# Kernel tuning notes

Hardware: AMD Instinct MI355X
Metric: run time of the kernel (lower is better)

Reference implementation:

```python
import jax, jax.numpy as jnp
import numpy as np
import math

K_HEADS = 16  # nb_heads from init_kwargs


def setup_inputs() -> dict:
    key = jax.random.key(0)
    ks = jax.random.split(key, 7)
    B, M, H, D = 2, 2048, 1024, 1024 // K_HEADS
    return {
        "h": jax.random.normal(ks[0], (B, M, H), jnp.float32),
        "h_cache": jax.random.normal(ks[1], (B, M, H), jnp.float32),
        "key_pe": jax.random.normal(ks[2], (1, D, M), jnp.float32),
        "Wq": jax.random.normal(ks[3], (H, H), jnp.float32) * 0.02,
        "Wk": jax.random.normal(ks[4], (H, H), jnp.float32) * 0.02,
        "Wv": jax.random.normal(ks[5], (H, H), jnp.float32) * 0.02,
        "Wo": jax.random.normal(ks[6], (H, H), jnp.float32) * 0.02,
    }


def _heads(x, K):
    # [B, M, H] -> [B, K, M, D]
    B, M, H = x.shape
    return x.reshape(B, M, K, H // K).transpose(0, 2, 1, 3)


def reference(h, h_cache, key_pe, Wq, Wk, Wv, Wo):
    B, M, H = h.shape
    K = K_HEADS
    D = H // K
    q = _heads(h @ Wq.T, K)        # [B, K, M, D]
    k = _heads(h_cache @ Wk.T, K)  # [B, K, L, D], L == M
    v = _heads(h_cache @ Wv.T, K)  # [B, K, L, D]

    attn_cont = jnp.einsum("bkmd,bkld->bkml", q, k)            # content scores
    attn_pos = jnp.einsum("bkmd,dl->bkml", q, key_pe[0])       # positional scores
    attn = (attn_cont + attn_pos[..., :M]) / math.sqrt(D)
    attn = jax.nn.softmax(attn, axis=-1)  # computed as in source, but source
    # (faithfully) multiplies VALUE by attn_cont, not attn:
    out = jnp.einsum("bkml,bkld->bkmd", attn_cont, v)          # [B, K, M, D]
    out = out.transpose(0, 2, 1, 3).reshape(B, M, H)
    return out @ Wo.T
```

## Files before the change

kernel.cpp:

```cpp
#include <hip/hip_runtime.h>
#include <hip/hip_bf16.h>

#define BB 2
#define MM 2048
#define HH 1024
#define KH 16

typedef short s16x8 __attribute__((ext_vector_type(8)));
typedef float f32x4 __attribute__((ext_vector_type(4)));
typedef float f32x16 __attribute__((ext_vector_type(16)));

#define GLOBAL_AS __attribute__((address_space(1)))
#define LDS_AS    __attribute__((address_space(3)))

__device__ __forceinline__ void async_copy16(const void* g, void* l) {
    __builtin_amdgcn_global_load_lds((const GLOBAL_AS void*)g, (LDS_AS void*)l, 16, 0, 0);
}

struct __align__(8) bf16x4_t { __hip_bfloat16 x, y, z, w; };

__global__ __launch_bounds__(256) void cvt_all(
    const float* __restrict__ h_f, const float* __restrict__ hc_f,
    const float* __restrict__ Wk_f, const float* __restrict__ Wv_f,
    const float* __restrict__ Wo_f, const float* __restrict__ Wq_f,
    __hip_bfloat16* __restrict__ hb, __hip_bfloat16* __restrict__ hcT,
    __hip_bfloat16* __restrict__ wkb, __hip_bfloat16* __restrict__ wvb,
    __hip_bfloat16* __restrict__ wob, __hip_bfloat16* __restrict__ wqt,
    float* __restrict__ Sz)
{
    __shared__ float Tl[64][65];
    const int seg = blockIdx.y;
    const int t = threadIdx.x;
    const int bx = blockIdx.x;

    if (seg == 1) {
        if (bx >= BB * 512) return;
        const int b = bx >> 9;
        const int tile = bx & 511;
        const int m0 = (tile >> 4) * 64;
        const int k0 = (tile & 15) * 64;
        const int r = t >> 6;
        const int c = t & 63;
        const float* src = hc_f + (size_t)b * MM * HH;
#pragma unroll
        for (int i = 0; i < 64; i += 4)
            Tl[r + i][c] = src[(size_t)(m0 + r + i) * HH + k0 + c];
        __syncthreads();
        __hip_bfloat16* dst = hcT + (size_t)b * HH * MM;
        const int ml = (t & 15) * 4;
#pragma unroll
        for (int ii = 0; ii < 4; ++ii) {
            const int kl = (t >> 4) + 16 * ii;
            bf16x4_t o;
            o.x = __float2bfloat16(Tl[ml + 0][kl]);
            o.y = __float2bfloat16(Tl[ml + 1][kl]);
            o.z = __float2bfloat16(Tl[ml + 2][kl]);
            o.w = __float2bfloat16(Tl[ml + 3][kl]);
            *(bf16x4_t*)(dst + (size_t)(k0 + kl) * MM + m0 + ml) = o;
        }
        return;
    }
    if (seg == 5) {
        if (bx < 128) {
            const int i = (bx * 256 + t) * 4;
            float4 z = {0.f, 0.f, 0.f, 0.f};
            *(float4*)(Sz + i) = z;
            return;
        }
        if (bx >= 384) return;
        const int tile = bx - 128;
        const int j0 = (tile >> 4) * 64;
        const int k0 = (tile & 15) * 64;
        const int r = t >> 6;
        const int c = t & 63;
#pragma unroll
        for (int i = 0; i < 64; i += 4)
            Tl[r + i][c] = Wq_f[(size_t)(j0 + r + i) * HH + k0 + c];
        __syncthreads();
        const int ml = (t & 15) * 4;
#pragma unroll
        for (int ii = 0; ii < 4; ++ii) {
            const int kl = (t >> 4) + 16 * ii;
            bf16x4_t o;
            o.x = __float2bfloat16(Tl[ml + 0][kl]);
            o.y = __float2bfloat16(Tl[ml + 1][kl]);
            o.z = __float2bfloat16(Tl[ml + 2][kl]);
            o.w = __float2bfloat16(Tl[ml + 3][kl]);
            *(bf16x4_t*)(wqt + (size_t)(k0 + kl) * HH + j0 + ml) = o;
        }
        return;
    }
    const float* src;
    __hip_bfloat16* dst;
    int n;
    switch (seg) {
        case 0: src = h_f;  dst = hb;  n = BB * MM * HH; break;
        case 2: src = Wk_f; dst = wkb; n = HH * HH; break;
        case 3: src = Wv_f; dst = wvb; n = HH * HH; break;
        default: src = Wo_f; dst = wob; n = HH * HH; break;
    }
    const int i = (bx * 256 + t) * 4;
    if (i + 3 < n) {
        const float4 v = *(const float4*)(src + i);
        bf16x4_t o;
        o.x = __float2bfloat16(v.x);
        o.y = __float2bfloat16(v.y);
        o.z = __float2bfloat16(v.z);
        o.w = __float2bfloat16(v.w);
        *(bf16x4_t*)(dst + i) = o;
    }
}

__device__ __forceinline__ void store_c(__hip_bfloat16* C, size_t idx, float v) {
    C[idx] = __float2bfloat16(v);
}
__device__ __forceinline__ void store_c(float* C, size_t idx, float v) { C[idx] = v; }

__device__ __forceinline__ f32x16 nt64x2_acc(
    const __hip_bfloat16* __restrict__ A, const __hip_bfloat16* __restrict__ B,
    int kd, size_t ld, __hip_bfloat16* As, __hip_bfloat16* Bs)
{
    const int t    = threadIdx.x;
    const int lane = t & 63;
    const int wave = t >> 6;
    const int srow = lane >> 3;
    const int sw   = ((lane & 7) ^ srow) * 8;
    const int wm   = (wave >> 1) * 32;
    const int wn   = (wave & 1) * 32;
    const int fm   = lane & 31;
    const int fm7  = fm & 7;
    const int ghi  = lane >> 5;

    f32x16 acc = {};
    for (int k0 = 0; k0 < kd; k0 += 128) {
        __syncthreads();
#pragma unroll
        for (int h = 0; h < 2; ++h)
#pragma unroll
            for (int i = 0; i < 2; ++i) {
                const int c = wave * 2 + i;
                async_copy16(A + (size_t)(c * 8 + srow) * ld + k0 + 64 * h + sw,
                             As + h * 4096 + c * 512);
                async_copy16(B + (size_t)(c * 8 + srow) * ld + k0 + 64 * h + sw,
                             Bs + h * 4096 + c * 512);
            }
        __syncthreads();
#pragma unroll
        for (int h = 0; h < 2; ++h)
#pragma unroll
            for (int ks = 0; ks < 64; ks += 16) {
                const int pos = ((((ks >> 3) + ghi) ^ fm7) * 8);
                const s16x8 af = *(const s16x8*)(As + h * 4096 + (wm + fm) * 64 + pos);
                const s16x8 bf = *(const s16x8*)(Bs + h * 4096 + (wn + fm) * 64 + pos);
                acc = __builtin_amdgcn_mfma_f32_32x32x16_bf16(af, bf, acc, 0, 0, 0);
            }
    }
    return acc;
}

template <typename OutT>
__device__ __forceinline__ void store_tile64(OutT* C, int ldc, const f32x16& acc) {
    const int lane = threadIdx.x & 63;
    const int wave = threadIdx.x >> 6;
    const int wm = (wave >> 1) * 32;
    const int wn = (wave & 1) * 32;
    const int col = wn + (lane & 31);
    const int rb  = 4 * (lane >> 5);
#pragma unroll
    for (int r = 0; r < 16; ++r) {
        const int row = wm + (r & 3) + 8 * (r >> 2) + rb;
        store_c(C, (size_t)row * ldc + col, acc[r]);
    }
}

__global__ __launch_bounds__(256) void gemm_g(
    const __hip_bfloat16* __restrict__ hcT, __hip_bfloat16* __restrict__ G)
{
    __shared__ __align__(16) char smem[32768];
    __hip_bfloat16* As = (__hip_bfloat16*)smem;
    __hip_bfloat16* Bs = (__hip_bfloat16*)(smem + 16384);
    __hip_bfloat16* Ts = (__hip_bfloat16*)smem;

    const int b = blockIdx.z;
    int i = 0, rem = blockIdx.x;
    while (rem >= 16 - i) { rem -= 16 - i; ++i; }
    const int j = i + rem;
    const int m0 = i * 64, n0 = j * 64;

    const __hip_bfloat16* Ab = hcT + (size_t)b * HH * MM;
    f32x16 acc = nt64x2_acc(Ab + (size_t)m0 * MM, Ab + (size_t)n0 * MM, MM, MM, As, Bs);

    __hip_bfloat16* Gb = G + (size_t)b * HH * HH;
    store_tile64(Gb + (size_t)m0 * HH + n0, HH, acc);

    if (i == j) return;

    __syncthreads();
    {
        const int lane = threadIdx.x & 63;
        const int wave = threadIdx.x >> 6;
        const int wm = (wave >> 1) * 32;
        const int wn = (wave & 1) * 32;
        const int col = wn + (lane & 31);
        const int rb  = 4 * (lane >> 5);
#pragma unroll
        for (int r = 0; r < 16; ++r) {
            const int row = wm + (r & 3) + 8 * (r >> 2) + rb;
            Ts[row * 72 + col] = __float2bfloat16(acc[r]);
        }
    }
    __syncthreads();
    {
        const int t = threadIdx.x;
        const int rp = t >> 2;
        const int c0 = (t & 3) * 16;
        __hip_bfloat16* dst = Gb + (size_t)(n0 + rp) * HH + m0 + c0;
#pragma unroll
        for (int kk = 0; kk < 4; ++kk) {
            bf16x4_t o;
            o.x = Ts[(c0 + 4 * kk + 0) * 72 + rp];
            o.y = Ts[(c0 + 4 * kk + 1) * 72 + rp];
            o.z = Ts[(c0 + 4 * kk + 2) * 72 + rp];
            o.w = Ts[(c0 + 4 * kk + 3) * 72 + rp];
            *(bf16x4_t*)(dst + 4 * kk) = o;
        }
    }
}

#define LPP 72

__global__ __launch_bounds__(256) void gemm_vt(
    const __hip_bfloat16* __restrict__ wkb, const __hip_bfloat16* __restrict__ wvb,
    const __hip_bfloat16* __restrict__ G, float* __restrict__ S)
{
    __shared__ __align__(16) char smem[32768];
    __hip_bfloat16* As = (__hip_bfloat16*)smem;
    __hip_bfloat16* Bs = (__hip_bfloat16*)(smem + 16384);
    __hip_bfloat16* Pl = (__hip_bfloat16*)smem;
    __hip_bfloat16* Wl = (__hip_bfloat16*)(smem + 64 * LPP * 2);

    const int t    = threadIdx.x;
    const int lane = t & 63;
    const int wave = t >> 6;
    const int kt   = blockIdx.x;
    const int head = blockIdx.y;
    const int b    = blockIdx.z;

    const __hip_bfloat16* Arow = G + (size_t)b * HH * HH + (size_t)kt * 64 * HH;
    const __hip_bfloat16* Brow = wkb + (size_t)head * 64 * HH;

    f32x16 acc = nt64x2_acc(Arow, Brow, HH, HH, As, Bs);
    __syncthreads();

    {
        const int wm = (wave >> 1) * 32;
        const int wn = (wave & 1) * 32;
        const int col_i = wn + (lane & 31);
        const int ghi4  = 4 * (lane >> 5);
#pragma unroll
        for (int g = 0; g < 4; ++g) {
            const int ccb = wm + 8 * g + ghi4;
            bf16x4_t o;
            o.x = __float2bfloat16(acc[4 * g + 0]);
            o.y = __float2bfloat16(acc[4 * g + 1]);
            o.z = __float2bfloat16(acc[4 * g + 2]);
            o.w = __float2bfloat16(acc[4 * g + 3]);
            *(bf16x4_t*)(Pl + col_i * LPP + ccb) = o;
        }
    }
    {
        const int srow = lane >> 3;
        const int sw   = ((lane & 7) ^ srow) * 8;
#pragma unroll
        for (int i = 0; i < 2; ++i) {
            const int c = wave * 2 + i;
            async_copy16(wvb + (size_t)(head * 64 + c * 8 + srow) * HH + kt * 64 + sw,
                         Wl + c * 512);
        }
    }
    __syncthreads();

    const int fr  = lane & 15;
    const int fq  = (lane >> 4) * 8;
    const int wm2 = wave * 16;

    f32x4 acc2[4] = {};
#pragma unroll
    for (int kk = 0; kk < 64; kk += 32) {
        const s16x8 af = *(const s16x8*)(Pl + (wm2 + fr) * LPP + kk + fq);
#pragma unroll
        for (int nj = 0; nj < 4; ++nj) {
            const int row = nj * 16 + fr;
            const s16x8 bfv = *(const s16x8*)(
                Wl + row * 64 + ((((kk + fq) >> 3) ^ (row & 7)) << 3));
            acc2[nj] = __builtin_amdgcn_mfma_f32_16x16x32_bf16(af, bfv, acc2[nj], 0, 0, 0);
        }
    }

    float* Sg = S + ((size_t)b * KH + head) * 4096;
    const int er = (lane >> 4) * 4;
    const int ec = lane & 15;
#pragma unroll
    for (int nj = 0; nj < 4; ++nj)
#pragma unroll
        for (int rr = 0; rr < 4; ++rr)
            atomicAdd(&Sg[(wm2 + er + rr) * 64 + nj * 16 + ec], acc2[nj][rr]);
}

__global__ __launch_bounds__(256) void gemm_f(
    const __hip_bfloat16* __restrict__ W2, const __hip_bfloat16* __restrict__ WqT,
    __hip_bfloat16* __restrict__ F)
{
    __shared__ __align__(16) char smem[32768];
    __hip_bfloat16* As = (__hip_bfloat16*)smem;
    __hip_bfloat16* Bs = (__hip_bfloat16*)(smem + 16384);
    const int b = blockIdx.z;
    const int m0 = blockIdx.x * 64, n0 = blockIdx.y * 64;
    f32x16 acc = nt64x2_acc(W2 + (size_t)b * HH * HH + (size_t)m0 * HH,
                            WqT + (size_t)n0 * HH, HH, HH, As, Bs);
    store_tile64(F + (size_t)b * HH * HH + (size_t)m0 * HH + n0, HH, acc);
}

__global__ __launch_bounds__(256) void gemm_final(
    const __hip_bfloat16* __restrict__ hb, const __hip_bfloat16* __restrict__ F,
    float* __restrict__ outg)
{
    __shared__ __align__(16) char smem[32768];
    __hip_bfloat16* As = (__hip_bfloat16*)smem;
    __hip_bfloat16* Bs = (__hip_bfloat16*)(smem + 16384);
    const int b = blockIdx.z;
    const int m0 = blockIdx.x * 64, n0 = blockIdx.y * 64;
    f32x16 acc = nt64x2_acc(hb + (size_t)b * MM * HH + (size_t)m0 * HH,
                            F + (size_t)b * HH * HH + (size_t)n0 * HH, HH, HH, As, Bs);
    store_tile64(outg + (size_t)b * MM * HH + (size_t)m0 * HH + n0, HH, acc);
}

__global__ __launch_bounds__(256) void w2_fold(
    const __hip_bfloat16* __restrict__ Wo,
    const float* __restrict__ S,
    __hip_bfloat16* __restrict__ W2)
{
    __shared__ float Sl[64 * 68];
    __shared__ float Wl[128 * 68];
    const int t = threadIdx.x, head = blockIdx.y, b = blockIdx.z;
    const int n0 = blockIdx.x * 128;

    const float* Sg = S + ((size_t)b * KH + head) * 4096;
    for (int idx = t; idx < 4096; idx += 256) {
        const int dp = idx >> 6, d = idx & 63;
        Sl[d * 68 + dp] = Sg[idx];
    }
    for (int idx = t; idx < 1024; idx += 256) {
        const int r = idx >> 3, c8 = (idx & 7) * 8;
        s16x8 wv = *(const s16x8*)(Wo + (size_t)(n0 + r) * HH + head * 64 + c8);
#pragma unroll
        for (int j = 0; j < 8; ++j) {
            __hip_bfloat16 wb = *(((const __hip_bfloat16*)&wv) + j);
            Wl[r * 68 + c8 + j] = __bfloat162float(wb);
        }
    }
    __syncthreads();

    const int dpb = (t & 15) * 4;
    const int ng  = t >> 4;
    float acc[8][4] = {};
    for (int d0 = 0; d0 < 64; d0 += 4) {
        f32x4 sv[4];
#pragma unroll
        for (int r = 0; r < 4; ++r)
            sv[r] = *(const f32x4*)(Sl + (d0 + r) * 68 + dpb);
#pragma unroll
        for (int i = 0; i < 8; ++i) {
            const f32x4 wv = *(const f32x4*)(Wl + (ng + 16 * i) * 68 + d0);
#pragma unroll
            for (int r = 0; r < 4; ++r)
#pragma unroll
                for (int j = 0; j < 4; ++j)
                    acc[i][j] += wv[r] * sv[r][j];
        }
    }

#pragma unroll
    for (int i = 0; i < 8; ++i) {
        bf16x4_t o;
        o.x = __float2bfloat16(acc[i][0]);
        o.y = __float2bfloat16(acc[i][1]);
        o.z = __float2bfloat16(acc[i][2]);
        o.w = __float2bfloat16(acc[i][3]);
        *(bf16x4_t*)(W2 + (size_t)b * HH * HH + (size_t)(n0 + ng + 16 * i) * HH
                     + head * 64 + dpb) = o;
    }
}

extern "C" void kernel_launch(void* const* d_in, const int* in_sizes, int n_in,
                              void* d_out, int out_size, void* d_ws, size_t ws_size,
                              hipStream_t stream) {
    const float* h_f  = (const float*)d_in[0];
    const float* hc_f = (const float*)d_in[1];
    const float* Wq_f = (const float*)d_in[3];
    const float* Wk_f = (const float*)d_in[4];
    const float* Wv_f = (const float*)d_in[5];
    const float* Wo_f = (const float*)d_in[6];
    float* out = (float*)d_out;

    const size_t act_b = (size_t)BB * MM * HH * 2;
    const size_t w_b   = (size_t)HH * HH * 2;
    char* ws = (char*)d_ws;
    __hip_bfloat16* hb   = (__hip_bfloat16*)(ws);
    __hip_bfloat16* hcT  = (__hip_bfloat16*)(ws + act_b);
    __hip_bfloat16* wkb  = (__hip_bfloat16*)(ws + 2 * act_b);
    __hip_bfloat16* wvb  = (__hip_bfloat16*)(ws + 2 * act_b + w_b);
    __hip_bfloat16* wob  = (__hip_bfloat16*)(ws + 2 * act_b + 2 * w_b);
    __hip_bfloat16* wqt  = (__hip_bfloat16*)(ws + 2 * act_b + 3 * w_b);
    __hip_bfloat16* Gb   = (__hip_bfloat16*)(ws + 2 * act_b + 4 * w_b);
    float*          Sbuf = (float*)(ws + 2 * act_b + 6 * w_b);
    __hip_bfloat16* W2   = (__hip_bfloat16*)(ws + 2 * act_b + 6 * w_b + (size_t)512 * 1024);
    __hip_bfloat16* Fbuf = (__hip_bfloat16*)(ws + 2 * act_b + 8 * w_b + (size_t)512 * 1024);

    const dim3 blk(256);

    cvt_all<<<dim3(4096, 6), blk, 0, stream>>>(h_f, hc_f, Wk_f, Wv_f, Wo_f, Wq_f,
                                               hb, hcT, wkb, wvb, wob, wqt, Sbuf);

    gemm_g<<<dim3(136, 1, BB), blk, 0, stream>>>(hcT, Gb);

    gemm_vt<<<dim3(16, KH, BB), blk, 0, stream>>>(wkb, wvb, Gb, Sbuf);

    w2_fold<<<dim3(8, KH, BB), blk, 0, stream>>>(wob, Sbuf, W2);

    gemm_f<<<dim3(16, 16, BB), blk, 0, stream>>>(W2, wqt, Fbuf);

    gemm_final<<<dim3(32, 16, BB), blk, 0, stream>>>(hb, Fbuf, out);
}
```

Baseline: 169.1 us.

## Double-buffer GEMM K loop, merge Q projection into Gram kernel, drop F GEMM

The shared GEMM helper now double-buffers 64-wide K slices in LDS. It prefetches the next slice while MFMAs consume the current one, replacing the previous load-then-compute pattern over 128-wide steps. The Q projection (h·Wq) is computed as extra blocks inside the Gram-matrix kernel, so it runs concurrently with G. The final output is then Q times W2 directly, which removes the separate W2·WqT GEMM, its launch, and the transposed Wq conversion. In exchange the final GEMM contracts over a bf16-rounded Q intermediate, and the mega kernel mixes two tile workloads of different K lengths.

```diff
diff --git a/kernel.cpp b/kernel.cpp
--- a/kernel.cpp
+++ b/kernel.cpp
@@ -25,7 +25,7 @@
     const float* __restrict__ Wo_f, const float* __restrict__ Wq_f,
     __hip_bfloat16* __restrict__ hb, __hip_bfloat16* __restrict__ hcT,
     __hip_bfloat16* __restrict__ wkb, __hip_bfloat16* __restrict__ wvb,
-    __hip_bfloat16* __restrict__ wob, __hip_bfloat16* __restrict__ wqt,
+    __hip_bfloat16* __restrict__ wob, __hip_bfloat16* __restrict__ wqb,
     float* __restrict__ Sz)
 {
     __shared__ float Tl[64][65];
@@ -34,59 +34,34 @@
     const int bx = blockIdx.x;
 
     if (seg == 1) {
-        if (bx >= BB * 512) return;
-        const int b = bx >> 9;
-        const int tile = bx & 511;
-        const int m0 = (tile >> 4) * 64;
-        const int k0 = (tile & 15) * 64;
-        const int r = t >> 6;
-        const int c = t & 63;
-        const float* src = hc_f + (size_t)b * MM * HH;
-#pragma unroll
-        for (int i = 0; i < 64; i += 4)
-            Tl[r + i][c] = src[(size_t)(m0 + r + i) * HH + k0 + c];
-        __syncthreads();
-        __hip_bfloat16* dst = hcT + (size_t)b * HH * MM;
-        const int ml = (t & 15) * 4;
-#pragma unroll
-        for (int ii = 0; ii < 4; ++ii) {
-            const int kl = (t >> 4) + 16 * ii;
-            bf16x4_t o;
-            o.x = __float2bfloat16(Tl[ml + 0][kl]);
-            o.y = __float2bfloat16(Tl[ml + 1][kl]);
-            o.z = __float2bfloat16(Tl[ml + 2][kl]);
-            o.w = __float2bfloat16(Tl[ml + 3][kl]);
-            *(bf16x4_t*)(dst + (size_t)(k0 + kl) * MM + m0 + ml) = o;
-        }
-        return;
-    }
-    if (seg == 5) {
-        if (bx < 128) {
-            const int i = (bx * 256 + t) * 4;
+        if (bx < BB * 512) {
+            const int b = bx >> 9;
+            const int tile = bx & 511;
+            const int m0 = (tile >> 4) * 64;
+            const int k0 = (tile & 15) * 64;
+            const int r = t >> 6;
+            const int c = t & 63;
+            const float* src = hc_f + (size_t)b * MM * HH;
+#pragma unroll
+            for (int i = 0; i < 64; i += 4)
+                Tl[r + i][c] = src[(size_t)(m0 + r + i) * HH + k0 + c];
+            __syncthreads();
+            __hip_bfloat16* dst = hcT + (size_t)b * HH * MM;
+            const int ml = (t & 15) * 4;
+#pragma unroll
+            for (int ii = 0; ii < 4; ++ii) {
+                const int kl = (t >> 4) + 16 * ii;
+                bf16x4_t o;
+                o.x = __float2bfloat16(Tl[ml + 0][kl]);
+                o.y = __float2bfloat16(Tl[ml + 1][kl]);
+                o.z = __float2bfloat16(Tl[ml + 2][kl]);
+                o.w = __float2bfloat16(Tl[ml + 3][kl]);
+                *(bf16x4_t*)(dst + (size_t)(k0 + kl) * MM + m0 + ml) = o;
+            }
+        } else if (bx < BB * 512 + 128) {
+            const int i = ((bx - BB * 512) * 256 + t) * 4;
             float4 z = {0.f, 0.f, 0.f, 0.f};
             *(float4*)(Sz + i) = z;
-            return;
-        }
-        if (bx >= 384) return;
-        const int tile = bx - 128;
-        const int j0 = (tile >> 4) * 64;
-        const int k0 = (tile & 15) * 64;
-        const int r = t >> 6;
-        const int c = t & 63;
-#pragma unroll
-        for (int i = 0; i < 64; i += 4)
-            Tl[r + i][c] = Wq_f[(size_t)(j0 + r + i) * HH + k0 + c];
-        __syncthreads();
-        const int ml = (t & 15) * 4;
-#pragma unroll
-        for (int ii = 0; ii < 4; ++ii) {
-            const int kl = (t >> 4) + 16 * ii;
-            bf16x4_t o;
-            o.x = __float2bfloat16(Tl[ml + 0][kl]);
-            o.y = __float2bfloat16(Tl[ml + 1][kl]);
-            o.z = __float2bfloat16(Tl[ml + 2][kl]);
-            o.w = __float2bfloat16(Tl[ml + 3][kl]);
-            *(bf16x4_t*)(wqt + (size_t)(k0 + kl) * HH + j0 + ml) = o;
         }
         return;
     }
@@ -97,7 +72,8 @@
         case 0: src = h_f;  dst = hb;  n = BB * MM * HH; break;
         case 2: src = Wk_f; dst = wkb; n = HH * HH; break;
         case 3: src = Wv_f; dst = wvb; n = HH * HH; break;
-        default: src = Wo_f; dst = wob; n = HH * HH; break;
+        case 4: src = Wo_f; dst = wob; n = HH * HH; break;
+        default: src = Wq_f; dst = wqb; n = HH * HH; break;
     }
     const int i = (bx * 256 + t) * 4;
     if (i + 3 < n) {
@@ -116,7 +92,7 @@
 }
 __device__ __forceinline__ void store_c(float* C, size_t idx, float v) { C[idx] = v; }
 
-__device__ __forceinline__ f32x16 nt64x2_acc(
+__device__ __forceinline__ f32x16 nt64_db_acc(
     const __hip_bfloat16* __restrict__ A, const __hip_bfloat16* __restrict__ B,
     int kd, size_t ld, __hip_bfloat16* As, __hip_bfloat16* Bs)
 {
@@ -131,29 +107,37 @@
     const int fm7  = fm & 7;
     const int ghi  = lane >> 5;
 
+#pragma unroll
+    for (int i = 0; i < 2; ++i) {
+        const int c = wave * 2 + i;
+        async_copy16(A + (size_t)(c * 8 + srow) * ld + sw, As + c * 512);
+        async_copy16(B + (size_t)(c * 8 + srow) * ld + sw, Bs + c * 512);
+    }
+    __syncthreads();
+
     f32x16 acc = {};
-    for (int k0 = 0; k0 < kd; k0 += 128) {
-        __syncthreads();
-#pragma unroll
-        for (int h = 0; h < 2; ++h)
+    int cur = 0;
+    for (int k0 = 0; k0 < kd; k0 += 64) {
+        const int nxt = cur ^ 1;
+        if (k0 + 64 < kd) {
 #pragma unroll
             for (int i = 0; i < 2; ++i) {
                 const int c = wave * 2 + i;
-                async_copy16(A + (size_t)(c * 8 + srow) * ld + k0 + 64 * h + sw,
-                             As + h * 4096 + c * 512);
-                async_copy16(B + (size_t)(c * 8 + srow) * ld + k0 + 64 * h + sw,
-                             Bs + h * 4096 + c * 512);
+                async_copy16(A + (size_t)(c * 8 + srow) * ld + (k0 + 64) + sw,
+                             As + nxt * 4096 + c * 512);
+                async_copy16(B + (size_t)(c * 8 + srow) * ld + (k0 + 64) + sw,
+                             Bs + nxt * 4096 + c * 512);
             }
+        }
+#pragma unroll
+        for (int ks = 0; ks < 64; ks += 16) {
+            const int pos = ((((ks >> 3) + ghi) ^ fm7) * 8);
+            const s16x8 af = *(const s16x8*)(As + cur * 4096 + (wm + fm) * 64 + pos);
+            const s16x8 bf = *(const s16x8*)(Bs + cur * 4096 + (wn + fm) * 64 + pos);
+            acc = __builtin_amdgcn_mfma_f32_32x32x16_bf16(af, bf, acc, 0, 0, 0);
+        }
         __syncthreads();
-#pragma unroll
-        for (int h = 0; h < 2; ++h)
-#pragma unroll
-            for (int ks = 0; ks < 64; ks += 16) {
-                const int pos = ((((ks >> 3) + ghi) ^ fm7) * 8);
-                const s16x8 af = *(const s16x8*)(As + h * 4096 + (wm + fm) * 64 + pos);
-                const s16x8 bf = *(const s16x8*)(Bs + h * 4096 + (wn + fm) * 64 + pos);
-                acc = __builtin_amdgcn_mfma_f32_32x32x16_bf16(af, bf, acc, 0, 0, 0);
-            }
+        cur = nxt;
     }
     return acc;
 }
@@ -173,8 +157,10 @@
     }
 }
 
-__global__ __launch_bounds__(256) void gemm_g(
-    const __hip_bfloat16* __restrict__ hcT, __hip_bfloat16* __restrict__ G)
+__global__ __launch_bounds__(256) void mega_gq(
+    const __hip_bfloat16* __restrict__ hb, const __hip_bfloat16* __restrict__ wqb,
+    const __hip_bfloat16* __restrict__ hcT,
+    __hip_bfloat16* __restrict__ qb, __hip_bfloat16* __restrict__ G)
 {
     __shared__ __align__(16) char smem[32768];
     __hip_bfloat16* As = (__hip_bfloat16*)smem;
@@ -182,13 +168,23 @@
     __hip_bfloat16* Ts = (__hip_bfloat16*)smem;
 
     const int b = blockIdx.z;
-    int i = 0, rem = blockIdx.x;
+    const int bx = blockIdx.x;
+
+    if (bx < 512) {
+        const int m0 = (bx >> 4) * 64, n0 = (bx & 15) * 64;
+        f32x16 acc = nt64_db_acc(hb + (size_t)b * MM * HH + (size_t)m0 * HH,
+                                 wqb + (size_t)n0 * HH, HH, HH, As, Bs);
+        store_tile64(qb + (size_t)b * MM * HH + (size_t)m0 * HH + n0, HH, acc);
+        return;
+    }
+
+    int i = 0, rem = bx - 512;
     while (rem >= 16 - i) { rem -= 16 - i; ++i; }
     const int j = i + rem;
     const int m0 = i * 64, n0 = j * 64;
 
     const __hip_bfloat16* Ab = hcT + (size_t)b * HH * MM;
-    f32x16 acc = nt64x2_acc(Ab + (size_t)m0 * MM, Ab + (size_t)n0 * MM, MM, MM, As, Bs);
+    f32x16 acc = nt64_db_acc(Ab + (size_t)m0 * MM, Ab + (size_t)n0 * MM, MM, MM, As, Bs);
 
     __hip_bfloat16* Gb = G + (size_t)b * HH * HH;
     store_tile64(Gb + (size_t)m0 * HH + n0, HH, acc);
@@ -249,7 +245,7 @@
     const __hip_bfloat16* Arow = G + (size_t)b * HH * HH + (size_t)kt * 64 * HH;
     const __hip_bfloat16* Brow = wkb + (size_t)head * 64 * HH;
 
-    f32x16 acc = nt64x2_acc(Arow, Brow, HH, HH, As, Bs);
+    f32x16 acc = nt64_db_acc(Arow, Brow, HH, HH, As, Bs);
     __syncthreads();
 
     {
@@ -307,31 +303,18 @@
             atomicAdd(&Sg[(wm2 + er + rr) * 64 + nj * 16 + ec], acc2[nj][rr]);
 }
 
-__global__ __launch_bounds__(256) void gemm_f(
-    const __hip_bfloat16* __restrict__ W2, const __hip_bfloat16* __restrict__ WqT,
-    __hip_bfloat16* __restrict__ F)
+__global__ __launch_bounds__(256) void gemm_final2(
+    const __hip_bfloat16* __restrict__ qb, const __hip_bfloat16* __restrict__ W2,
+    float* __restrict__ outg)
 {
     __shared__ __align__(16) char smem[32768];
     __hip_bfloat16* As = (__hip_bfloat16*)smem;
     __hip_bfloat16* Bs = (__hip_bfloat16*)(smem + 16384);
     const int b = blockIdx.z;
-    const int m0 = blockIdx.x * 64, n0 = blockIdx.y * 64;
-    f32x16 acc = nt64x2_acc(W2 + (size_t)b * HH * HH + (size_t)m0 * HH,
-                            WqT + (size_t)n0 * HH, HH, HH, As, Bs);
-    store_tile64(F + (size_t)b * HH * HH + (size_t)m0 * HH + n0, HH, acc);
-}
-
-__global__ __launch_bounds__(256) void gemm_final(
-    const __hip_bfloat16* __restrict__ hb, const __hip_bfloat16* __restrict__ F,
-    float* __restrict__ outg)
-{
-    __shared__ __align__(16) char smem[32768];
-    __hip_bfloat16* As = (__hip_bfloat16*)smem;
-    __hip_bfloat16* Bs = (__hip_bfloat16*)(smem + 16384);
-    const int b = blockIdx.z;
-    const int m0 = blockIdx.x * 64, n0 = blockIdx.y * 64;
-    f32x16 acc = nt64x2_acc(hb + (size_t)b * MM * HH + (size_t)m0 * HH,
-                            F + (size_t)b * HH * HH + (size_t)n0 * HH, HH, HH, As, Bs);
+    const int m0 = (blockIdx.x >> 4) * 64, n0 = (blockIdx.x & 15) * 64;
+    f32x16 acc = nt64_db_acc(qb + (size_t)b * MM * HH + (size_t)m0 * HH,
+                             W2 + (size_t)b * HH * HH + (size_t)n0 * HH,
+                             HH, HH, As, Bs);
     store_tile64(outg + (size_t)b * MM * HH + (size_t)m0 * HH + n0, HH, acc);
 }
 
@@ -411,24 +394,22 @@
     __hip_bfloat16* wkb  = (__hip_bfloat16*)(ws + 2 * act_b);
     __hip_bfloat16* wvb  = (__hip_bfloat16*)(ws + 2 * act_b + w_b);
     __hip_bfloat16* wob  = (__hip_bfloat16*)(ws + 2 * act_b + 2 * w_b);
-    __hip_bfloat16* wqt  = (__hip_bfloat16*)(ws + 2 * act_b + 3 * w_b);
-    __hip_bfloat16* Gb   = (__hip_bfloat16*)(ws + 2 * act_b + 4 * w_b);
-    float*          Sbuf = (float*)(ws + 2 * act_b + 6 * w_b);
-    __hip_bfloat16* W2   = (__hip_bfloat16*)(ws + 2 * act_b + 6 * w_b + (size_t)512 * 1024);
-    __hip_bfloat16* Fbuf = (__hip_bfloat16*)(ws + 2 * act_b + 8 * w_b + (size_t)512 * 1024);
+    __hip_bfloat16* wqb  = (__hip_bfloat16*)(ws + 2 * act_b + 3 * w_b);
+    __hip_bfloat16* qb   = (__hip_bfloat16*)(ws + 2 * act_b + 4 * w_b);
+    __hip_bfloat16* Gb   = (__hip_bfloat16*)(ws + 3 * act_b + 4 * w_b);
+    float*          Sbuf = (float*)(ws + 3 * act_b + 6 * w_b);
+    __hip_bfloat16* W2   = (__hip_bfloat16*)(ws + 3 * act_b + 6 * w_b + (size_t)512 * 1024);
 
     const dim3 blk(256);
 
     cvt_all<<<dim3(4096, 6), blk, 0, stream>>>(h_f, hc_f, Wk_f, Wv_f, Wo_f, Wq_f,
-                                               hb, hcT, wkb, wvb, wob, wqt, Sbuf);
-
-    gemm_g<<<dim3(136, 1, BB), blk, 0, stream>>>(hcT, Gb);
+                                               hb, hcT, wkb, wvb, wob, wqb, Sbuf);
+
+    mega_gq<<<dim3(648, 1, BB), blk, 0, stream>>>(hb, wqb, hcT, qb, Gb);
 
     gemm_vt<<<dim3(16, KH, BB), blk, 0, stream>>>(wkb, wvb, Gb, Sbuf);
 
     w2_fold<<<dim3(8, KH, BB), blk, 0, stream>>>(wob, Sbuf, W2);
 
-    gemm_f<<<dim3(16, 16, BB), blk, 0, stream>>>(W2, wqt, Fbuf);
-
-    gemm_final<<<dim3(32, 16, BB), blk, 0, stream>>>(hb, Fbuf, out);
-}
+    gemm_final2<<<dim3(512, 1, BB), blk, 0, stream>>>(qb, W2, out);
+}
```

Measured after the change: 170.9 us. About the same (+1.1%).
